# Optimization experiments

Measured on AMD Instinct MI355X. Metric: run time of the kernel, lower is better.

Reference implementation:

```python
import jax, jax.numpy as jnp
import numpy as np

TAU = 2.0          # spikingjelly LIFNode default tau
V_TH = 1.0         # v_threshold
SG_ALPHA = 4.0     # surrogate sigmoid alpha (default)
B, T, C, V = 128, 2048, 3, 1
H, L, NC = 192, 2, 12


@jax.custom_vjp
def spike_fn(u):
    # Heaviside on (v - v_th); surrogate sigmoid gradient in bwd
    return (u >= 0.0).astype(u.dtype)

def _spike_fwd(u):
    return spike_fn(u), u

def _spike_bwd(u, g):
    s = jax.nn.sigmoid(SG_ALPHA * u)
    return (g * SG_ALPHA * s * (1.0 - s),)

spike_fn.defvjp(_spike_fwd, _spike_bwd)


def setup_inputs() -> dict:
    key = jax.random.key(0)
    ks = jax.random.split(key, 8)
    in_dim = C * V
    sc = lambda d: 1.0 / np.sqrt(d)
    return {
        "x": jax.random.normal(ks[0], (B, T, C, V), dtype=jnp.float32),
        "W_in": jax.random.uniform(ks[1], (H, in_dim), jnp.float32, -sc(in_dim), sc(in_dim)),
        "b_in": jax.random.uniform(ks[2], (H,), jnp.float32, -sc(in_dim), sc(in_dim)),
        "W_cells": jax.random.uniform(ks[3], (L, H, H), jnp.float32, -sc(H), sc(H)),
        "b_cells": jax.random.uniform(ks[4], (L, H), jnp.float32, -sc(H), sc(H)),
        "W_head": jax.random.uniform(ks[5], (NC, H), jnp.float32, -sc(H), sc(H)),
        "b_head": jax.random.uniform(ks[6], (NC,), jnp.float32, -sc(H), sc(H)),
    }


def reference(x, W_in, b_in, W_cells, b_cells, W_head, b_head):
    b, t = x.shape[0], x.shape[1]
    xf = x.reshape(b, t, -1)                               # [B,T,in_dim]
    # in_proj applied to every timestep up-front (one big GEMM)
    z_all = jnp.einsum('btd,hd->tbh', xf, W_in) + b_in     # [T,B,H]

    def step(carry, z_in):
        h, v = carry                                       # each [L,B,H]
        z = z_in
        new_h, new_v = [], []
        for l in range(L):
            z = z + h[l] @ W_cells[l].T + b_cells[l]
            v_l = v[l] + (z - v[l]) / TAU                  # LIF charge (decay_input)
            s = spike_fn(v_l - V_TH)                       # fire
            v_l = v_l * (1.0 - s)                          # hard reset to 0
            new_h.append(s)
            new_v.append(v_l)
            z = s
        return (jnp.stack(new_h), jnp.stack(new_v)), z

    init = (jnp.zeros((L, b, H), x.dtype), jnp.zeros((L, b, H), x.dtype))
    _, readout = jax.lax.scan(step, init, z_all)           # [T,B,H]
    feat = readout.mean(axis=0)                            # [B,H]; dropout is identity at eval
    return feat @ W_head.T + b_head                        # [B,NC]
```

## Files before the change

kernel.cpp:

```cpp
#include <hip/hip_runtime.h>

#define HN 192
#define TT 2048
#define NCLS 12
#define ROWB 768
#define L0_PAD    147456
#define LDS_LIST0 149504
#define LDS_LIST1 150432
#define LDS_S0    151360
#define LDS_FEAT  152896
#define LDS_TOTAL 153664

__global__ void snn_pack_k(const float* __restrict__ Wc, float* __restrict__ ws) {
  int idx = blockIdx.x * 256 + threadIdx.x;
  if (idx < HN * HN) {
    int i = idx / HN, j = idx % HN;
    ws[j * HN + i] = Wc[idx];
  } else if (idx < 2 * HN * HN) {
    int r = idx - HN * HN;
    int i = r / HN, j = r % HN;
    ws[(193 + j) * HN + i] = Wc[idx];
  } else {
    int r = idx - 2 * HN * HN;
    if (r < HN) ws[192 * HN + r] = 0.0f;
    if (r < 256) ws[385 * HN + r] = 0.0f;
  }
}

__device__ __forceinline__ float4 add4(float4 a, float4 b) {
  return make_float4(a.x + b.x, a.y + b.y, a.z + b.z, a.w + b.w);
}
__device__ __forceinline__ int lanecnt_lt(unsigned long long m) {
  return __builtin_amdgcn_mbcnt_hi((unsigned)(m >> 32),
           __builtin_amdgcn_mbcnt_lo((unsigned)m, 0u));
}

#define READC(da, db, base, c) do { \
  da = *(const int4*)((base) + (c) * 32); \
  db = *(const int4*)((base) + (c) * 32 + 16); } while (0)

#define ISS8Q(p, ca, cb, basep) do { \
  p##0 = *(const float4*)((basep) + (unsigned)(ca).x + ln16); \
  p##1 = *(const float4*)((basep) + (unsigned)(ca).y + ln16); \
  p##2 = *(const float4*)((basep) + (unsigned)(ca).z + ln16); \
  p##3 = *(const float4*)((basep) + (unsigned)(ca).w + ln16); \
  p##4 = *(const float4*)((basep) + (unsigned)(cb).x + ln16); \
  p##5 = *(const float4*)((basep) + (unsigned)(cb).y + ln16); \
  p##6 = *(const float4*)((basep) + (unsigned)(cb).z + ln16); \
  p##7 = *(const float4*)((basep) + (unsigned)(cb).w + ln16); } while (0)

#define CONS8Q(acc, p) acc = add4(acc, \
  add4(add4(add4(p##0, p##1), add4(p##2, p##3)), \
       add4(add4(p##4, p##5), add4(p##6, p##7))))

__global__ __launch_bounds__(128, 1) void snn_main_k(
    const float* __restrict__ x, const float* __restrict__ W_in,
    const float* __restrict__ b_in, const float* __restrict__ b_cells,
    const float* __restrict__ W_head, const float* __restrict__ b_head,
    const float* __restrict__ ws, float* __restrict__ out)
{
  extern __shared__ char lds[];
  const int tid = threadIdx.x;
  const int ln  = tid & 63;
  const bool isW0 = (tid < 64);
  const int b   = blockIdx.x;
  const unsigned ln16 = (unsigned)ln << 4;
  const char* ldsb = lds;
  char* list0b = lds + LDS_LIST0;
  char* list1b = lds + LDS_LIST1;
  float* feat  = (float*)(lds + LDS_FEAT);
  const char* w1zb = (const char*)ws + 192 * ROWB;

  {
    const float4* src = (const float4*)ws;
    float4* dst = (float4*)lds;
    for (int i = tid; i < (192 * ROWB) / 16; i += 128) dst[i] = src[i];
    ((float4*)(lds + L0_PAD))[tid] = make_float4(0.f, 0.f, 0.f, 0.f);
  }
  __syncthreads();

  int vz;
  asm volatile("v_mov_b32 %0, 0" : "=v"(vz));

  float wi0[4], wi1[4], wi2[4], zb[4], b1z[4];
  #pragma unroll
  for (int k = 0; k < 4; ++k) {
    int i = 4 * ln + k;
    bool a = (i < HN);
    int ii = a ? i : 0;
    wi0[k] = a ? W_in[ii * 3 + 0] : 0.f;
    wi1[k] = a ? W_in[ii * 3 + 1] : 0.f;
    wi2[k] = a ? W_in[ii * 3 + 2] : 0.f;
    zb[k]  = a ? (b_in[ii] + b_cells[ii]) : -1e30f;
    b1z[k] = a ? b_cells[HN + ii] : -1e30f;
  }
  const float* __restrict__ xb = x + (size_t)b * TT * 3;
  const int vo = ln * 3072;

  float v0k[4] = {0, 0, 0, 0};
  int n0 = 0;
  int4 c0a = {0,0,0,0}, c0b = {0,0,0,0}, c1a = {0,0,0,0}, c1b = {0,0,0,0};
  float x0 = xb[vz + 0], x1 = xb[vz + 1], x2 = xb[vz + 2];
  float v1k[4] = {0, 0, 0, 0}, cntk[4] = {0, 0, 0, 0};
  int ngl = 0;
  float4 gA0, gA1, gA2, gA3, gA4, gA5, gA6, gA7;
  float4 gB0, gB1, gB2, gB3, gB4, gB5, gB6, gB7;
  gA0=gA1=gA2=gA3=gA4=gA5=gA6=gA7=make_float4(0.f,0.f,0.f,0.f);
  gB0=gB1=gB2=gB3=gB4=gB5=gB6=gB7=gA0;

  #pragma unroll 1
  for (int i = 0; i <= TT; ++i) {
    if (isW0) {
      if (i < TT) {
        const int wp = i & 1;
        const int ngr0 = (n0 + 7) >> 3;
        float4 a0v = make_float4(0.f, 0.f, 0.f, 0.f);
        float4 hA0, hA1, hA2, hA3, hA4, hA5, hA6, hA7;
        float4 hB0, hB1, hB2, hB3, hB4, hB5, hB6, hB7;
        if (ngr0 > 0) ISS8Q(hA, c0a, c0b, ldsb);
        if (ngr0 > 1) ISS8Q(hB, c1a, c1b, ldsb);
        float zh[4];
        #pragma unroll
        for (int k = 0; k < 4; ++k)
          zh[k] = (x0 * wi0[k] + x1 * wi1[k] + x2 * wi2[k] + zb[k]) * 0.5f
                + v0k[k] * 0.5f;
        const int tn = (i + 1 < TT) ? i + 1 : 0;
        const float nx0 = xb[tn * 3 + vz + 0];
        const float nx1 = xb[tn * 3 + vz + 1];
        const float nx2 = xb[tn * 3 + vz + 2];
        if (ngr0 > 0) CONS8Q(a0v, hA);
        if (ngr0 > 1) CONS8Q(a0v, hB);
        if (ngr0 > 2) {
          #pragma unroll 1
          for (int g = 2; g < ngr0; ++g) {
            int4 ea, eb;
            READC(ea, eb, list0b, g);
            float4 r0, r1, r2, r3, r4, r5, r6, r7;
            ISS8Q(r, ea, eb, ldsb);
            CONS8Q(a0v, r);
          }
        }
        const float a0arr[4] = {a0v.x, a0v.y, a0v.z, a0v.w};
        float s0f[4];
        unsigned long long mm0, mm1, mm2, mm3;
        {
          float v;
          v = zh[0] + a0arr[0] * 0.5f; bool s0 = (v >= 1.0f);
          mm0 = __ballot(s0 ? 1 : 0); s0f[0] = s0 ? 1.0f : 0.0f; v0k[0] = s0 ? 0.0f : v;
          v = zh[1] + a0arr[1] * 0.5f; bool s1 = (v >= 1.0f);
          mm1 = __ballot(s1 ? 1 : 0); s0f[1] = s1 ? 1.0f : 0.0f; v0k[1] = s1 ? 0.0f : v;
          v = zh[2] + a0arr[2] * 0.5f; bool s2 = (v >= 1.0f);
          mm2 = __ballot(s2 ? 1 : 0); s0f[2] = s2 ? 1.0f : 0.0f; v0k[2] = s2 ? 0.0f : v;
          v = zh[3] + a0arr[3] * 0.5f; bool s3 = (v >= 1.0f);
          mm3 = __ballot(s3 ? 1 : 0); s0f[3] = s3 ? 1.0f : 0.0f; v0k[3] = s3 ? 0.0f : v;
        }
        if (ln < 48)
          *(float4*)(lds + LDS_S0 + wp * 768 + ln16) =
              make_float4(s0f[0], s0f[1], s0f[2], s0f[3]);
        const int q0   = (int)__popcll(mm0);
        const int q01  = q0  + (int)__popcll(mm1);
        const int q012 = q01 + (int)__popcll(mm2);
        const int p0n  = q012 + (int)__popcll(mm3);
        if (s0f[0] != 0.f) *(int*)(list0b + 4 * lanecnt_lt(mm0)) = vo;
        if (s0f[1] != 0.f) *(int*)(list0b + 4 * (q0   + lanecnt_lt(mm1))) = vo + ROWB;
        if (s0f[2] != 0.f) *(int*)(list0b + 4 * (q01  + lanecnt_lt(mm2))) = vo + 2 * ROWB;
        if (s0f[3] != 0.f) *(int*)(list0b + 4 * (q012 + lanecnt_lt(mm3))) = vo + 3 * ROWB;
        if (ln < 8) *(int*)(list0b + 4 * (p0n + ln)) = L0_PAD;
        n0 = p0n;
        asm volatile("" ::: "memory");
        READC(c0a, c0b, list0b, 0);
        READC(c1a, c1b, list0b, 1);
        asm volatile("s_waitcnt lgkmcnt(4)" ::: "memory");
        x0 = nx0; x1 = nx1; x2 = nx2;
      }
    } else {
      if (i > 0) {
        const int rp = (i - 1) & 1;
        const float4 s0v = *(const float4*)(lds + LDS_S0 + rp * 768 + ln16);
        float4 a1v = make_float4(0.f, 0.f, 0.f, 0.f);
        if (ngl > 0) CONS8Q(a1v, gA);
        if (ngl > 1) CONS8Q(a1v, gB);
        if (ngl > 2) {
          #pragma unroll 1
          for (int og = 2; og < ngl; ++og) {
            int4 ea, eb;
            READC(ea, eb, list1b, og);
            float4 r0, r1, r2, r3, r4, r5, r6, r7;
            ISS8Q(r, ea, eb, w1zb);
            CONS8Q(a1v, r);
          }
        }
        const float a1arr[4] = {a1v.x, a1v.y, a1v.z, a1v.w};
        const float s0a[4] = {s0v.x, s0v.y, s0v.z, s0v.w};
        float s1w[4];
        unsigned long long nn0, nn1, nn2, nn3;
        {
          float u, v;
          u = b1z[0] + a1arr[0] + s0a[0]; v = v1k[0] + (u - v1k[0]) * 0.5f;
          bool s0 = (v >= 1.0f); nn0 = __ballot(s0 ? 1 : 0);
          s1w[0] = s0 ? 1.0f : 0.0f; v1k[0] = s0 ? 0.0f : v;
          u = b1z[1] + a1arr[1] + s0a[1]; v = v1k[1] + (u - v1k[1]) * 0.5f;
          bool s1 = (v >= 1.0f); nn1 = __ballot(s1 ? 1 : 0);
          s1w[1] = s1 ? 1.0f : 0.0f; v1k[1] = s1 ? 0.0f : v;
          u = b1z[2] + a1arr[2] + s0a[2]; v = v1k[2] + (u - v1k[2]) * 0.5f;
          bool s2 = (v >= 1.0f); nn2 = __ballot(s2 ? 1 : 0);
          s1w[2] = s2 ? 1.0f : 0.0f; v1k[2] = s2 ? 0.0f : v;
          u = b1z[3] + a1arr[3] + s0a[3]; v = v1k[3] + (u - v1k[3]) * 0.5f;
          bool s3 = (v >= 1.0f); nn3 = __ballot(s3 ? 1 : 0);
          s1w[3] = s3 ? 1.0f : 0.0f; v1k[3] = s3 ? 0.0f : v;
        }
        cntk[0] += s1w[0]; cntk[1] += s1w[1]; cntk[2] += s1w[2]; cntk[3] += s1w[3];
        const int r0c  = (int)__popcll(nn0);
        const int r01  = r0c + (int)__popcll(nn1);
        const int r012 = r01 + (int)__popcll(nn2);
        const int p1n  = r012 + (int)__popcll(nn3);
        if (s1w[0] != 0.f) *(int*)(list1b + 4 * lanecnt_lt(nn0)) = vo + ROWB;
        if (s1w[1] != 0.f) *(int*)(list1b + 4 * (r0c  + lanecnt_lt(nn1))) = vo + 2 * ROWB;
        if (s1w[2] != 0.f) *(int*)(list1b + 4 * (r01  + lanecnt_lt(nn2))) = vo + 3 * ROWB;
        if (s1w[3] != 0.f) *(int*)(list1b + 4 * (r012 + lanecnt_lt(nn3))) = vo + 4 * ROWB;
        if (ln < 8) *(int*)(list1b + 4 * (p1n + ln)) = 0;
        if (i < TT) {
          int4 d0a, d0b, d1a, d1b;
          READC(d0a, d0b, list1b, 0);
          READC(d1a, d1b, list1b, 1);
          const int ng1 = (p1n + 7) >> 3;
          if (ng1 > 0) ISS8Q(gA, d0a, d0b, w1zb);
          if (ng1 > 1) ISS8Q(gB, d1a, d1b, w1zb);
          ngl = ng1;
        }
      }
    }
    asm volatile("" ::: "memory");
    __builtin_amdgcn_s_barrier();
    __builtin_amdgcn_sched_barrier(0);
    asm volatile("" ::: "memory");
  }

  __syncthreads();
  if (!isW0 && ln < 48) {
    const float r = 1.0f / 2048.0f;
    ((float4*)feat)[ln] = make_float4(cntk[0] * r, cntk[1] * r, cntk[2] * r, cntk[3] * r);
  }
  __syncthreads();
  if (tid < NCLS) {
    float a = b_head[tid];
    const float* wh = W_head + tid * HN;
    #pragma unroll 8
    for (int q = 0; q < HN; ++q) a += feat[q] * wh[q];
    out[b * NCLS + tid] = a;
  }
}

extern "C" void kernel_launch(void* const* d_in, const int* in_sizes, int n_in,
                              void* d_out, int out_size, void* d_ws, size_t ws_size,
                              hipStream_t stream) {
  const float* x       = (const float*)d_in[0];
  const float* W_in    = (const float*)d_in[1];
  const float* b_in    = (const float*)d_in[2];
  const float* W_cells = (const float*)d_in[3];
  const float* b_cells = (const float*)d_in[4];
  const float* W_head  = (const float*)d_in[5];
  const float* b_head  = (const float*)d_in[6];
  float* out = (float*)d_out;
  float* ws  = (float*)d_ws;

  snn_pack_k<<<(2 * HN * HN + 512 + 255) / 256, 256, 0, stream>>>(W_cells, ws);
  snn_main_k<<<128, 128, LDS_TOTAL, stream>>>(
      x, W_in, b_in, b_cells, W_head, b_head, ws, out);
}
```

Before: 1.024 ms.

## Process two batch rows per workgroup to interleave independent recurrences

Each workgroup now runs two batch elements (A and B) through the two-layer spiking recurrence at the same time, halving the grid to 64 blocks. Interleaving two independent dependency chains per wave is meant to hide LDS and global load latency that a single serial recurrence leaves exposed. The spike-list writes also become branchless by sending non-spiking lanes to a junk slot, and overflow gather groups are partly unrolled. The cost is higher register pressure, more LDS, and using only 64 of the GPU's compute units, so the per-step critical path grows.

```diff
diff --git a/kernel.cpp b/kernel.cpp
--- a/kernel.cpp
+++ b/kernel.cpp
@@ -5,11 +5,15 @@
 #define NCLS 12
 #define ROWB 768
 #define L0_PAD    147456
-#define LDS_LIST0 149504
-#define LDS_LIST1 150432
-#define LDS_S0    151360
-#define LDS_FEAT  152896
-#define LDS_TOTAL 153664
+#define LIST0A    149504
+#define LIST0B    150784
+#define LIST1A    152064
+#define LIST1B    153344
+#define S0A       154624
+#define S0B       156160
+#define FEATA     157696
+#define FEATB     158464
+#define LDS_TOTAL 159232
 
 __global__ void snn_pack_k(const float* __restrict__ Wc, float* __restrict__ ws) {
   int idx = blockIdx.x * 256 + threadIdx.x;
@@ -53,6 +57,80 @@
   add4(add4(add4(p##0, p##1), add4(p##2, p##3)), \
        add4(add4(p##4, p##5), add4(p##6, p##7))))
 
+#define OVF(nX, listB, accv, basep) \
+  if (nX > 16) { \
+    int4 ea_, eb_; \
+    float4 r0, r1, r2, r3, r4, r5, r6, r7; \
+    READC(ea_, eb_, listB, 2); \
+    ISS8Q(r, ea_, eb_, basep); \
+    CONS8Q(accv, r); \
+    if (nX > 24) { READC(ea_, eb_, listB, 3); ISS8Q(r, ea_, eb_, basep); CONS8Q(accv, r); } \
+    if (nX > 32) { \
+      _Pragma("unroll 1") \
+      for (int g_ = 4; g_ * 8 < nX; ++g_) { \
+        READC(ea_, eb_, listB, g_); ISS8Q(r, ea_, eb_, basep); CONS8Q(accv, r); } \
+    } \
+  }
+
+#define LIF0_BLOCK(zarr, a0v, v0k, s0f, pout, listB, s0dst) do { \
+  const float a0arr_[4] = {(a0v).x, (a0v).y, (a0v).z, (a0v).w}; \
+  bool s0_, s1_, s2_, s3_; \
+  unsigned long long m0_, m1_, m2_, m3_; \
+  { float u_, v_; \
+    u_ = zarr[0] + a0arr_[0]; v_ = v0k[0] + (u_ - v0k[0]) * 0.5f; \
+    s0_ = (v_ >= 1.0f); m0_ = __ballot(s0_ ? 1 : 0); \
+    s0f[0] = s0_ ? 1.0f : 0.0f; v0k[0] = s0_ ? 0.0f : v_; \
+    u_ = zarr[1] + a0arr_[1]; v_ = v0k[1] + (u_ - v0k[1]) * 0.5f; \
+    s1_ = (v_ >= 1.0f); m1_ = __ballot(s1_ ? 1 : 0); \
+    s0f[1] = s1_ ? 1.0f : 0.0f; v0k[1] = s1_ ? 0.0f : v_; \
+    u_ = zarr[2] + a0arr_[2]; v_ = v0k[2] + (u_ - v0k[2]) * 0.5f; \
+    s2_ = (v_ >= 1.0f); m2_ = __ballot(s2_ ? 1 : 0); \
+    s0f[2] = s2_ ? 1.0f : 0.0f; v0k[2] = s2_ ? 0.0f : v_; \
+    u_ = zarr[3] + a0arr_[3]; v_ = v0k[3] + (u_ - v0k[3]) * 0.5f; \
+    s3_ = (v_ >= 1.0f); m3_ = __ballot(s3_ ? 1 : 0); \
+    s0f[3] = s3_ ? 1.0f : 0.0f; v0k[3] = s3_ ? 0.0f : v_; } \
+  if (ln < 48) *(float4*)(s0dst) = make_float4(s0f[0], s0f[1], s0f[2], s0f[3]); \
+  const int q0_   = (int)__popcll(m0_); \
+  const int q01_  = q0_  + (int)__popcll(m1_); \
+  const int q012_ = q01_ + (int)__popcll(m2_); \
+  pout = q012_ + (int)__popcll(m3_); \
+  const int jk_ = 256 + ln; int s_; \
+  s_ = s0_ ? lanecnt_lt(m0_)           : jk_; *(int*)((listB) + 4 * s_) = vo; \
+  s_ = s1_ ? (q0_   + lanecnt_lt(m1_)) : jk_; *(int*)((listB) + 4 * s_) = vo + ROWB; \
+  s_ = s2_ ? (q01_  + lanecnt_lt(m2_)) : jk_; *(int*)((listB) + 4 * s_) = vo + 2 * ROWB; \
+  s_ = s3_ ? (q012_ + lanecnt_lt(m3_)) : jk_; *(int*)((listB) + 4 * s_) = vo + 3 * ROWB; \
+  *(int*)((listB) + 4 * (pout + ln)) = L0_PAD; \
+} while (0)
+
+#define LIF1_BLOCK(a1arr, v1k, cntk, pout, listB) do { \
+  bool s0_, s1_, s2_, s3_; \
+  unsigned long long m0_, m1_, m2_, m3_; \
+  float w_; \
+  { float u_, v_; \
+    u_ = b1z[0] + a1arr[0]; v_ = v1k[0] + (u_ - v1k[0]) * 0.5f; \
+    s0_ = (v_ >= 1.0f); m0_ = __ballot(s0_ ? 1 : 0); \
+    w_ = s0_ ? 1.0f : 0.0f; cntk[0] += w_; v1k[0] = s0_ ? 0.0f : v_; \
+    u_ = b1z[1] + a1arr[1]; v_ = v1k[1] + (u_ - v1k[1]) * 0.5f; \
+    s1_ = (v_ >= 1.0f); m1_ = __ballot(s1_ ? 1 : 0); \
+    w_ = s1_ ? 1.0f : 0.0f; cntk[1] += w_; v1k[1] = s1_ ? 0.0f : v_; \
+    u_ = b1z[2] + a1arr[2]; v_ = v1k[2] + (u_ - v1k[2]) * 0.5f; \
+    s2_ = (v_ >= 1.0f); m2_ = __ballot(s2_ ? 1 : 0); \
+    w_ = s2_ ? 1.0f : 0.0f; cntk[2] += w_; v1k[2] = s2_ ? 0.0f : v_; \
+    u_ = b1z[3] + a1arr[3]; v_ = v1k[3] + (u_ - v1k[3]) * 0.5f; \
+    s3_ = (v_ >= 1.0f); m3_ = __ballot(s3_ ? 1 : 0); \
+    w_ = s3_ ? 1.0f : 0.0f; cntk[3] += w_; v1k[3] = s3_ ? 0.0f : v_; } \
+  const int q0_   = (int)__popcll(m0_); \
+  const int q01_  = q0_  + (int)__popcll(m1_); \
+  const int q012_ = q01_ + (int)__popcll(m2_); \
+  pout = q012_ + (int)__popcll(m3_); \
+  const int jk_ = 256 + ln; int s_; \
+  s_ = s0_ ? lanecnt_lt(m0_)           : jk_; *(int*)((listB) + 4 * s_) = vo + ROWB; \
+  s_ = s1_ ? (q0_   + lanecnt_lt(m1_)) : jk_; *(int*)((listB) + 4 * s_) = vo + 2 * ROWB; \
+  s_ = s2_ ? (q01_  + lanecnt_lt(m2_)) : jk_; *(int*)((listB) + 4 * s_) = vo + 3 * ROWB; \
+  s_ = s3_ ? (q012_ + lanecnt_lt(m3_)) : jk_; *(int*)((listB) + 4 * s_) = vo + 4 * ROWB; \
+  *(int*)((listB) + 4 * (pout + ln)) = 0; \
+} while (0)
+
 __global__ __launch_bounds__(128, 1) void snn_main_k(
     const float* __restrict__ x, const float* __restrict__ W_in,
     const float* __restrict__ b_in, const float* __restrict__ b_cells,
@@ -63,12 +141,14 @@
   const int tid = threadIdx.x;
   const int ln  = tid & 63;
   const bool isW0 = (tid < 64);
-  const int b   = blockIdx.x;
+  const int bA  = 2 * blockIdx.x;
+  const int bB  = bA + 1;
   const unsigned ln16 = (unsigned)ln << 4;
   const char* ldsb = lds;
-  char* list0b = lds + LDS_LIST0;
-  char* list1b = lds + LDS_LIST1;
-  float* feat  = (float*)(lds + LDS_FEAT);
+  char* list0Ab = lds + LIST0A;
+  char* list0Bb = lds + LIST0B;
+  char* list1Ab = lds + LIST1A;
+  char* list1Bb = lds + LIST1B;
   const char* w1zb = (const char*)ws + 192 * ROWB;
 
   {
@@ -94,140 +174,110 @@
     zb[k]  = a ? (b_in[ii] + b_cells[ii]) : -1e30f;
     b1z[k] = a ? b_cells[HN + ii] : -1e30f;
   }
-  const float* __restrict__ xb = x + (size_t)b * TT * 3;
+  const float* __restrict__ xbA = x + (size_t)bA * TT * 3;
+  const float* __restrict__ xbB = x + (size_t)bB * TT * 3;
   const int vo = ln * 3072;
 
-  float v0k[4] = {0, 0, 0, 0};
-  int n0 = 0;
-  int4 c0a = {0,0,0,0}, c0b = {0,0,0,0}, c1a = {0,0,0,0}, c1b = {0,0,0,0};
-  float x0 = xb[vz + 0], x1 = xb[vz + 1], x2 = xb[vz + 2];
-  float v1k[4] = {0, 0, 0, 0}, cntk[4] = {0, 0, 0, 0};
-  int ngl = 0;
-  float4 gA0, gA1, gA2, gA3, gA4, gA5, gA6, gA7;
-  float4 gB0, gB1, gB2, gB3, gB4, gB5, gB6, gB7;
-  gA0=gA1=gA2=gA3=gA4=gA5=gA6=gA7=make_float4(0.f,0.f,0.f,0.f);
-  gB0=gB1=gB2=gB3=gB4=gB5=gB6=gB7=gA0;
+  float v0A[4] = {0, 0, 0, 0}, v0B[4] = {0, 0, 0, 0};
+  int nA = 0, nB = 0;
+  int4 cA0a = {L0_PAD,L0_PAD,L0_PAD,L0_PAD}, cA0b = cA0a, cA1a = cA0a, cA1b = cA0a;
+  int4 cB0a = cA0a, cB0b = cA0a, cB1a = cA0a, cB1b = cA0a;
+  float xA0 = xbA[vz + 0], xA1 = xbA[vz + 1], xA2 = xbA[vz + 2];
+  float xB0 = xbB[vz + 0], xB1 = xbB[vz + 1], xB2 = xbB[vz + 2];
+  float v1A[4] = {0, 0, 0, 0}, cntA[4] = {0, 0, 0, 0};
+  float v1B[4] = {0, 0, 0, 0}, cntB[4] = {0, 0, 0, 0};
+  int n1A = 0, n1B = 0;
+  float4 gAA0,gAA1,gAA2,gAA3,gAA4,gAA5,gAA6,gAA7;
+  float4 gBA0,gBA1,gBA2,gBA3,gBA4,gBA5,gBA6,gBA7;
+  float4 gAB0,gAB1,gAB2,gAB3,gAB4,gAB5,gAB6,gAB7;
+  float4 gBB0,gBB1,gBB2,gBB3,gBB4,gBB5,gBB6,gBB7;
+  if (!isW0) {
+    int4 dz = {0, 0, 0, 0};
+    ISS8Q(gAA, dz, dz, w1zb);
+    ISS8Q(gAB, dz, dz, w1zb);
+    gBA0=gBA1=gBA2=gBA3=gBA4=gBA5=gBA6=gBA7=make_float4(0.f,0.f,0.f,0.f);
+    gBB0=gBB1=gBB2=gBB3=gBB4=gBB5=gBB6=gBB7=gBA0;
+  }
 
   #pragma unroll 1
   for (int i = 0; i <= TT; ++i) {
     if (isW0) {
       if (i < TT) {
         const int wp = i & 1;
-        const int ngr0 = (n0 + 7) >> 3;
-        float4 a0v = make_float4(0.f, 0.f, 0.f, 0.f);
-        float4 hA0, hA1, hA2, hA3, hA4, hA5, hA6, hA7;
-        float4 hB0, hB1, hB2, hB3, hB4, hB5, hB6, hB7;
-        if (ngr0 > 0) ISS8Q(hA, c0a, c0b, ldsb);
-        if (ngr0 > 1) ISS8Q(hB, c1a, c1b, ldsb);
-        float zh[4];
+        float4 a0vA = make_float4(0.f, 0.f, 0.f, 0.f), a0vB = a0vA;
+        float4 hAA0,hAA1,hAA2,hAA3,hAA4,hAA5,hAA6,hAA7;
+        float4 hBA0,hBA1,hBA2,hBA3,hBA4,hBA5,hBA6,hBA7;
+        float4 hAB0,hAB1,hAB2,hAB3,hAB4,hAB5,hAB6,hAB7;
+        float4 hBB0,hBB1,hBB2,hBB3,hBB4,hBB5,hBB6,hBB7;
+        ISS8Q(hAA, cA0a, cA0b, ldsb);
+        if (nA > 8) ISS8Q(hBA, cA1a, cA1b, ldsb);
+        ISS8Q(hAB, cB0a, cB0b, ldsb);
+        if (nB > 8) ISS8Q(hBB, cB1a, cB1b, ldsb);
+        float zA[4], zB[4];
         #pragma unroll
-        for (int k = 0; k < 4; ++k)
-          zh[k] = (x0 * wi0[k] + x1 * wi1[k] + x2 * wi2[k] + zb[k]) * 0.5f
-                + v0k[k] * 0.5f;
+        for (int k = 0; k < 4; ++k) {
+          zA[k] = xA0 * wi0[k] + xA1 * wi1[k] + xA2 * wi2[k] + zb[k];
+          zB[k] = xB0 * wi0[k] + xB1 * wi1[k] + xB2 * wi2[k] + zb[k];
+        }
         const int tn = (i + 1 < TT) ? i + 1 : 0;
-        const float nx0 = xb[tn * 3 + vz + 0];
-        const float nx1 = xb[tn * 3 + vz + 1];
-        const float nx2 = xb[tn * 3 + vz + 2];
-        if (ngr0 > 0) CONS8Q(a0v, hA);
-        if (ngr0 > 1) CONS8Q(a0v, hB);
-        if (ngr0 > 2) {
-          #pragma unroll 1
-          for (int g = 2; g < ngr0; ++g) {
-            int4 ea, eb;
-            READC(ea, eb, list0b, g);
-            float4 r0, r1, r2, r3, r4, r5, r6, r7;
-            ISS8Q(r, ea, eb, ldsb);
-            CONS8Q(a0v, r);
-          }
-        }
-        const float a0arr[4] = {a0v.x, a0v.y, a0v.z, a0v.w};
-        float s0f[4];
-        unsigned long long mm0, mm1, mm2, mm3;
-        {
-          float v;
-          v = zh[0] + a0arr[0] * 0.5f; bool s0 = (v >= 1.0f);
-          mm0 = __ballot(s0 ? 1 : 0); s0f[0] = s0 ? 1.0f : 0.0f; v0k[0] = s0 ? 0.0f : v;
-          v = zh[1] + a0arr[1] * 0.5f; bool s1 = (v >= 1.0f);
-          mm1 = __ballot(s1 ? 1 : 0); s0f[1] = s1 ? 1.0f : 0.0f; v0k[1] = s1 ? 0.0f : v;
-          v = zh[2] + a0arr[2] * 0.5f; bool s2 = (v >= 1.0f);
-          mm2 = __ballot(s2 ? 1 : 0); s0f[2] = s2 ? 1.0f : 0.0f; v0k[2] = s2 ? 0.0f : v;
-          v = zh[3] + a0arr[3] * 0.5f; bool s3 = (v >= 1.0f);
-          mm3 = __ballot(s3 ? 1 : 0); s0f[3] = s3 ? 1.0f : 0.0f; v0k[3] = s3 ? 0.0f : v;
-        }
-        if (ln < 48)
-          *(float4*)(lds + LDS_S0 + wp * 768 + ln16) =
-              make_float4(s0f[0], s0f[1], s0f[2], s0f[3]);
-        const int q0   = (int)__popcll(mm0);
-        const int q01  = q0  + (int)__popcll(mm1);
-        const int q012 = q01 + (int)__popcll(mm2);
-        const int p0n  = q012 + (int)__popcll(mm3);
-        if (s0f[0] != 0.f) *(int*)(list0b + 4 * lanecnt_lt(mm0)) = vo;
-        if (s0f[1] != 0.f) *(int*)(list0b + 4 * (q0   + lanecnt_lt(mm1))) = vo + ROWB;
-        if (s0f[2] != 0.f) *(int*)(list0b + 4 * (q01  + lanecnt_lt(mm2))) = vo + 2 * ROWB;
-        if (s0f[3] != 0.f) *(int*)(list0b + 4 * (q012 + lanecnt_lt(mm3))) = vo + 3 * ROWB;
-        if (ln < 8) *(int*)(list0b + 4 * (p0n + ln)) = L0_PAD;
-        n0 = p0n;
+        const float nxA0 = xbA[tn * 3 + vz + 0];
+        const float nxA1 = xbA[tn * 3 + vz + 1];
+        const float nxA2 = xbA[tn * 3 + vz + 2];
+        const float nxB0 = xbB[tn * 3 + vz + 0];
+        const float nxB1 = xbB[tn * 3 + vz + 1];
+        const float nxB2 = xbB[tn * 3 + vz + 2];
+        CONS8Q(a0vA, hAA);
+        if (nA > 8) CONS8Q(a0vA, hBA);
+        OVF(nA, list0Ab, a0vA, ldsb);
+        CONS8Q(a0vB, hAB);
+        if (nB > 8) CONS8Q(a0vB, hBB);
+        OVF(nB, list0Bb, a0vB, ldsb);
+        float s0fA[4], s0fB[4];
+        int pA, pB;
+        LIF0_BLOCK(zA, a0vA, v0A, s0fA, pA, list0Ab, lds + S0A + wp * 768 + ln16);
+        LIF0_BLOCK(zB, a0vB, v0B, s0fB, pB, list0Bb, lds + S0B + wp * 768 + ln16);
+        nA = pA; nB = pB;
         asm volatile("" ::: "memory");
-        READC(c0a, c0b, list0b, 0);
-        READC(c1a, c1b, list0b, 1);
-        asm volatile("s_waitcnt lgkmcnt(4)" ::: "memory");
-        x0 = nx0; x1 = nx1; x2 = nx2;
+        READC(cA0a, cA0b, list0Ab, 0);
+        READC(cA1a, cA1b, list0Ab, 1);
+        READC(cB0a, cB0b, list0Bb, 0);
+        READC(cB1a, cB1b, list0Bb, 1);
+        asm volatile("s_waitcnt lgkmcnt(8)" ::: "memory");
+        xA0 = nxA0; xA1 = nxA1; xA2 = nxA2;
+        xB0 = nxB0; xB1 = nxB1; xB2 = nxB2;
       }
     } else {
       if (i > 0) {
         const int rp = (i - 1) & 1;
-        const float4 s0v = *(const float4*)(lds + LDS_S0 + rp * 768 + ln16);
-        float4 a1v = make_float4(0.f, 0.f, 0.f, 0.f);
-        if (ngl > 0) CONS8Q(a1v, gA);
-        if (ngl > 1) CONS8Q(a1v, gB);
-        if (ngl > 2) {
-          #pragma unroll 1
-          for (int og = 2; og < ngl; ++og) {
-            int4 ea, eb;
-            READC(ea, eb, list1b, og);
-            float4 r0, r1, r2, r3, r4, r5, r6, r7;
-            ISS8Q(r, ea, eb, w1zb);
-            CONS8Q(a1v, r);
-          }
+        const float4 s0vA = *(const float4*)(lds + S0A + rp * 768 + ln16);
+        const float4 s0vB = *(const float4*)(lds + S0B + rp * 768 + ln16);
+        float4 a1vA = make_float4(0.f, 0.f, 0.f, 0.f), a1vB = a1vA;
+        CONS8Q(a1vA, gAA);
+        if (n1A > 8) CONS8Q(a1vA, gBA);
+        OVF(n1A, list1Ab, a1vA, w1zb);
+        CONS8Q(a1vB, gAB);
+        if (n1B > 8) CONS8Q(a1vB, gBB);
+        OVF(n1B, list1Bb, a1vB, w1zb);
+        const float a1A[4] = {a1vA.x + s0vA.x, a1vA.y + s0vA.y,
+                              a1vA.z + s0vA.z, a1vA.w + s0vA.w};
+        const float a1B[4] = {a1vB.x + s0vB.x, a1vB.y + s0vB.y,
+                              a1vB.z + s0vB.z, a1vB.w + s0vB.w};
+        int pA, pB;
+        LIF1_BLOCK(a1A, v1A, cntA, pA, list1Ab);
+        LIF1_BLOCK(a1B, v1B, cntB, pB, list1Bb);
+        if (i < TT) {
+          int4 dA0a, dA0b, dA1a, dA1b, dB0a, dB0b, dB1a, dB1b;
+          asm volatile("" ::: "memory");
+          READC(dA0a, dA0b, list1Ab, 0);
+          READC(dA1a, dA1b, list1Ab, 1);
+          READC(dB0a, dB0b, list1Bb, 0);
+          READC(dB1a, dB1b, list1Bb, 1);
+          ISS8Q(gAA, dA0a, dA0b, w1zb);
+          if (pA > 8) ISS8Q(gBA, dA1a, dA1b, w1zb);
+          ISS8Q(gAB, dB0a, dB0b, w1zb);
+          if (pB > 8) ISS8Q(gBB, dB1a, dB1b, w1zb);
         }
-        const float a1arr[4] = {a1v.x, a1v.y, a1v.z, a1v.w};
-        const float s0a[4] = {s0v.x, s0v.y, s0v.z, s0v.w};
-        float s1w[4];
-        unsigned long long nn0, nn1, nn2, nn3;
-        {
-          float u, v;
-          u = b1z[0] + a1arr[0] + s0a[0]; v = v1k[0] + (u - v1k[0]) * 0.5f;
-          bool s0 = (v >= 1.0f); nn0 = __ballot(s0 ? 1 : 0);
-          s1w[0] = s0 ? 1.0f : 0.0f; v1k[0] = s0 ? 0.0f : v;
-          u = b1z[1] + a1arr[1] + s0a[1]; v = v1k[1] + (u - v1k[1]) * 0.5f;
-          bool s1 = (v >= 1.0f); nn1 = __ballot(s1 ? 1 : 0);
-          s1w[1] = s1 ? 1.0f : 0.0f; v1k[1] = s1 ? 0.0f : v;
-          u = b1z[2] + a1arr[2] + s0a[2]; v = v1k[2] + (u - v1k[2]) * 0.5f;
-          bool s2 = (v >= 1.0f); nn2 = __ballot(s2 ? 1 : 0);
-          s1w[2] = s2 ? 1.0f : 0.0f; v1k[2] = s2 ? 0.0f : v;
-          u = b1z[3] + a1arr[3] + s0a[3]; v = v1k[3] + (u - v1k[3]) * 0.5f;
-          bool s3 = (v >= 1.0f); nn3 = __ballot(s3 ? 1 : 0);
-          s1w[3] = s3 ? 1.0f : 0.0f; v1k[3] = s3 ? 0.0f : v;
-        }
-        cntk[0] += s1w[0]; cntk[1] += s1w[1]; cntk[2] += s1w[2]; cntk[3] += s1w[3];
-        const int r0c  = (int)__popcll(nn0);
-        const int r01  = r0c + (int)__popcll(nn1);
-        const int r012 = r01 + (int)__popcll(nn2);
-        const int p1n  = r012 + (int)__popcll(nn3);
-        if (s1w[0] != 0.f) *(int*)(list1b + 4 * lanecnt_lt(nn0)) = vo + ROWB;
-        if (s1w[1] != 0.f) *(int*)(list1b + 4 * (r0c  + lanecnt_lt(nn1))) = vo + 2 * ROWB;
-        if (s1w[2] != 0.f) *(int*)(list1b + 4 * (r01  + lanecnt_lt(nn2))) = vo + 3 * ROWB;
-        if (s1w[3] != 0.f) *(int*)(list1b + 4 * (r012 + lanecnt_lt(nn3))) = vo + 4 * ROWB;
-        if (ln < 8) *(int*)(list1b + 4 * (p1n + ln)) = 0;
-        if (i < TT) {
-          int4 d0a, d0b, d1a, d1b;
-          READC(d0a, d0b, list1b, 0);
-          READC(d1a, d1b, list1b, 1);
-          const int ng1 = (p1n + 7) >> 3;
-          if (ng1 > 0) ISS8Q(gA, d0a, d0b, w1zb);
-          if (ng1 > 1) ISS8Q(gB, d1a, d1b, w1zb);
-          ngl = ng1;
-        }
+        n1A = pA; n1B = pB;
       }
     }
     asm volatile("" ::: "memory");
@@ -239,15 +289,25 @@
   __syncthreads();
   if (!isW0 && ln < 48) {
     const float r = 1.0f / 2048.0f;
-    ((float4*)feat)[ln] = make_float4(cntk[0] * r, cntk[1] * r, cntk[2] * r, cntk[3] * r);
+    ((float4*)(lds + FEATA))[ln] = make_float4(cntA[0]*r, cntA[1]*r, cntA[2]*r, cntA[3]*r);
+    ((float4*)(lds + FEATB))[ln] = make_float4(cntB[0]*r, cntB[1]*r, cntB[2]*r, cntB[3]*r);
   }
   __syncthreads();
   if (tid < NCLS) {
+    const float* fA = (const float*)(lds + FEATA);
     float a = b_head[tid];
     const float* wh = W_head + tid * HN;
     #pragma unroll 8
-    for (int q = 0; q < HN; ++q) a += feat[q] * wh[q];
-    out[b * NCLS + tid] = a;
+    for (int q = 0; q < HN; ++q) a += fA[q] * wh[q];
+    out[bA * NCLS + tid] = a;
+  } else if (tid >= 64 && tid < 64 + NCLS) {
+    const int c = tid - 64;
+    const float* fB = (const float*)(lds + FEATB);
+    float a = b_head[c];
+    const float* wh = W_head + c * HN;
+    #pragma unroll 8
+    for (int q = 0; q < HN; ++q) a += fB[q] * wh[q];
+    out[bB * NCLS + c] = a;
   }
 }
 
@@ -265,6 +325,6 @@
   float* ws  = (float*)d_ws;
 
   snn_pack_k<<<(2 * HN * HN + 512 + 255) / 256, 256, 0, stream>>>(W_cells, ws);
-  snn_main_k<<<128, 128, LDS_TOTAL, stream>>>(
+  snn_main_k<<<64, 128, LDS_TOTAL, stream>>>(
       x, W_in, b_in, b_cells, W_head, b_head, ws, out);
 }
```

New measurement: 1.643 ms. 1.6x slower.
